# Kernel optimization log

Hardware: AMD Instinct MI355X
Metric: run time of the kernel (lower is better)

Reference implementation:

```python
import jax, jax.numpy as jnp
import numpy as np

B, N, IN_C = 8, 2048, 256
HEADS, OUT_C = 4, 128
E = 65536
BN_EPS = 1e-5


def setup_inputs() -> dict:
    key = jax.random.key(0)
    k1, k2, k3, k4 = jax.random.split(key, 4)
    x = jax.random.normal(k1, (B, N, IN_C), dtype=jnp.float32)
    edge_index = jax.random.randint(k2, (2, E), 0, N, dtype=jnp.int64)
    # Linear W: in_channels -> heads*out_channels, no bias (stored as [in, out])
    W = jax.random.normal(k3, (IN_C, HEADS * OUT_C), dtype=jnp.float32) / np.sqrt(IN_C)
    # att Linear: 2*out_channels -> 1, no bias (stored as a vector)
    a = jax.random.normal(k4, (2 * OUT_C,), dtype=jnp.float32) / np.sqrt(2 * OUT_C)
    bn_gamma = jnp.ones((OUT_C,), dtype=jnp.float32)
    bn_beta = jnp.zeros((OUT_C,), dtype=jnp.float32)
    return {"x": x, "edge_index": edge_index, "W": W, "a": a,
            "bn_gamma": bn_gamma, "bn_beta": bn_beta}


def reference(x, edge_index, W, a, bn_gamma, bn_beta):
    Bsz, Nn, _ = x.shape
    src, dst = edge_index[0], edge_index[1]
    h = (x @ W).reshape(Bsz, Nn, HEADS, OUT_C)  # [B,N,H,C]
    # att([h_src, h_dst]) == h_src @ a[:C] + h_dst @ a[C:] ; precompute per node
    s_src = jnp.einsum("bnhc,c->bnh", h, a[:OUT_C])  # [B,N,H]
    s_dst = jnp.einsum("bnhc,c->bnh", h, a[OUT_C:])
    e = s_src[:, src] + s_dst[:, dst]                 # [B,E,H]
    e = jax.nn.leaky_relu(e, negative_slope=0.2)
    e_avg = e.mean(axis=-1)                           # [B,E]
    # dense N x N attention: rows = dst, cols = src, -inf elsewhere
    attn = jnp.full((Bsz, Nn, Nn), -jnp.inf, dtype=x.dtype)
    attn = attn.at[:, dst, src].set(e_avg)
    attn = jax.nn.softmax(attn, axis=-1)
    attn = jnp.nan_to_num(attn, nan=0.0)              # rows with no edges -> 0
    # dropout is identity in eval mode
    h_flat = h.reshape(Bsz, Nn, HEADS * OUT_C)
    h_out = attn @ h_flat                             # [B,N,H*C]
    h_out = h_out.reshape(Bsz, Nn, HEADS, OUT_C).mean(axis=2)  # [B,N,C]
    # BatchNorm1d over channel dim (batch stats, biased var, affine params)
    mean = h_out.mean(axis=(0, 1))
    var = h_out.var(axis=(0, 1))
    h_out = (h_out - mean) / jnp.sqrt(var + BN_EPS) * bn_gamma + bn_beta
    return jax.nn.elu(h_out)
```

## Files before the change

### kernel.cpp

```cpp
#include <hip/hip_runtime.h>
#include <hip/hip_bf16.h>
#include <math.h>

#define BB 8
#define NN 2048
#define INC 256
#define CC 128
#define NE 65536
#define CAP 128
#define MROWS (BB*NN)
#define BN_EPS 1e-5f
#define NT 9
#define NKC 8
#define NFRAG (NT*NKC*64)

typedef unsigned int uint32;
typedef unsigned long long u64;
typedef __attribute__((ext_vector_type(8))) short short8;
typedef __attribute__((ext_vector_type(4))) float f32x4;

__device__ inline ushort f2bf(float f) {
  __hip_bfloat16 b = __float2bfloat16(f);
  return reinterpret_cast<ushort&>(b);
}
__device__ inline float bf2f(ushort h) {
  return __uint_as_float(((uint32)h) << 16);
}

__device__ inline void load_edge(const void* ei, int is64, int e, int& s, int& d) {
  if (is64) {
    const long long* p = (const long long*)ei;
    s = (int)p[e]; d = (int)p[NE + e];
  } else {
    const int* p = (const int*)ei;
    s = p[e]; d = p[NE + e];
  }
}

__global__ __launch_bounds__(256) void k_prep(const float* __restrict__ W,
                                              const float* __restrict__ a,
                                              const int* __restrict__ ei32,
                                              uint4* __restrict__ pack,
                                              int* __restrict__ flag,
                                              int* __restrict__ row_cnt) {
  __shared__ float Wl[8][520];
  __shared__ float Wms[8][132];
  __shared__ float Was[8][8];
  __shared__ float av[256];
  int m = blockIdx.x, tid = threadIdx.x;
  if (m < 8) row_cnt[m * 256 + tid] = 0;
  if (m == 0 && tid == 0) {
    int nz = 0;
    for (int t = 1; t < 128; t += 2) nz |= (ei32[t] != 0);
    *flag = nz ? 0 : 1;
  }
  av[tid] = a[tid];
  const float4* Wg = (const float4*)(W + (size_t)m * 8 * 512);
  #pragma unroll
  for (int i = 0; i < 4; ++i) {
    int idx = tid + i * 256;
    int r = idx >> 7, c4 = idx & 127;
    *(float4*)&Wl[r][c4 * 4] = Wg[idx];
  }
  __syncthreads();
  {
    int c = tid & 127, half = tid >> 7;
    #pragma unroll
    for (int ii = 0; ii < 4; ++ii) {
      int r = half * 4 + ii;
      Wms[r][c] = 0.25f * (Wl[r][c] + Wl[r][128 + c] + Wl[r][256 + c] + Wl[r][384 + c]);
    }
  }
  {
    int i8 = tid >> 5, c2 = tid & 31;
    float p[8];
    #pragma unroll
    for (int j = 0; j < 8; ++j) p[j] = 0.0f;
    #pragma unroll
    for (int t4 = 0; t4 < 4; ++t4) {
      int cc = c2 + t4 * 32;
      float asrc = av[cc], adst = av[128 + cc];
      #pragma unroll
      for (int h = 0; h < 4; ++h) {
        float w = Wl[i8][h * 128 + cc];
        p[h] += w * asrc;
        p[4 + h] += w * adst;
      }
    }
    #pragma unroll
    for (int off = 16; off > 0; off >>= 1)
      #pragma unroll
      for (int j = 0; j < 8; ++j) p[j] += __shfl_xor(p[j], off, 64);
    if (c2 < 8) Was[i8][c2] = p[c2];
  }
  __syncthreads();
  if (tid < 144) {
    int t = tid >> 4, l16 = tid & 15;
    int cch = t * 16 + l16;
    int kc = m >> 2, g = m & 3;
    uint32 h[8];
    #pragma unroll
    for (int j = 0; j < 8; ++j) {
      float v = 0.0f;
      if (cch < CC) v = Wms[j][cch];
      else if (cch < CC + 8) v = Was[j][cch - CC];
      h[j] = (uint32)f2bf(v);
    }
    uint4 u;
    u.x = h[0] | (h[1] << 16);
    u.y = h[2] | (h[3] << 16);
    u.z = h[4] | (h[5] << 16);
    u.w = h[6] | (h[7] << 16);
    pack[(t * NKC + kc) * 64 + g * 16 + l16] = u;
  }
}

__global__ __launch_bounds__(512) void k_gemm(const float* __restrict__ x,
                                              const uint4* __restrict__ pack,
                                              const void* __restrict__ ei,
                                              const int* __restrict__ flag,
                                              ushort* __restrict__ hm,
                                              float* __restrict__ s,
                                              int* __restrict__ row_cnt,
                                              int* __restrict__ row_src) {
  __shared__ uint4 lp[NFRAG];
  int tid = threadIdx.x;
  if (tid < 256) {
    int e = blockIdx.x * 256 + tid;
    int is64 = *flag;
    int src, dst;
    load_edge(ei, is64, e, src, dst);
    int pos = atomicAdd(&row_cnt[dst], 1);
    if (pos < CAP) row_src[dst * CAP + pos] = src;
  }
  #pragma unroll
  for (int i = 0; i < 9; ++i) lp[i * 512 + tid] = pack[i * 512 + tid];

  int lane = tid & 63, wv = tid >> 6;
  int rt = wv & 3, th = wv >> 2;
  int g = lane >> 4;
  int xrow = blockIdx.x * 64 + rt * 16 + (lane & 15);
  const float* xr = x + (size_t)xrow * INC;

  short8 xf[8];
  #pragma unroll
  for (int kc = 0; kc < 8; ++kc) {
    f32x4 xa = *(const f32x4*)(xr + kc * 32 + g * 8);
    f32x4 xb = *(const f32x4*)(xr + kc * 32 + g * 8 + 4);
    short8 t;
    t[0] = (short)f2bf(xa[0]); t[1] = (short)f2bf(xa[1]);
    t[2] = (short)f2bf(xa[2]); t[3] = (short)f2bf(xa[3]);
    t[4] = (short)f2bf(xb[0]); t[5] = (short)f2bf(xb[1]);
    t[6] = (short)f2bf(xb[2]); t[7] = (short)f2bf(xb[3]);
    xf[kc] = t;
  }
  __syncthreads();

  f32x4 acc[4];
  f32x4 accE = (f32x4)(0.0f);
  #pragma unroll
  for (int i = 0; i < 4; ++i) acc[i] = (f32x4)(0.0f);

  const short8* fr = (const short8*)lp;
  int tb = th * 4;
  #pragma unroll
  for (int kc = 0; kc < NKC; ++kc) {
    #pragma unroll
    for (int i = 0; i < 4; ++i) {
      short8 af = fr[((tb + i) * NKC + kc) * 64 + lane];
      acc[i] = __builtin_amdgcn_mfma_f32_16x16x32_bf16(af, xf[kc], acc[i], 0, 0, 0);
    }
    short8 ae = fr[(8 * NKC + kc) * 64 + lane];
    accE = __builtin_amdgcn_mfma_f32_16x16x32_bf16(ae, xf[kc], accE, 0, 0, 0);
  }

  ushort* hrow = hm + (size_t)xrow * CC;
  #pragma unroll
  for (int i = 0; i < 4; ++i) {
    int t = tb + i;
    uint32 p0 = (uint32)f2bf(acc[i][0]) | ((uint32)f2bf(acc[i][1]) << 16);
    uint32 p1 = (uint32)f2bf(acc[i][2]) | ((uint32)f2bf(acc[i][3]) << 16);
    *(uint2*)(hrow + t * 16 + g * 4) = make_uint2(p0, p1);
  }
  if (th == 1 && g < 2) {
    int b = xrow >> 11, n = xrow & (NN - 1);
    *(f32x4*)(s + ((size_t)n * BB + b) * 8 + g * 4) = accE;
  }
}

__global__ __launch_bounds__(256) void k_agg(const int* __restrict__ row_cnt,
                                             const int* __restrict__ row_src,
                                             const float* __restrict__ s,
                                             const uint32* __restrict__ hm32,
                                             uint32* __restrict__ hout,
                                             f32x4* __restrict__ part) {
  __shared__ int rsrc[CAP], csrc[CAP];
  __shared__ float swgt[8][CAP];
  __shared__ float emat[8][CAP];
  __shared__ float sdl[8][4];
  __shared__ f32x4 red[256];
  __shared__ uint32 bmask[64];
  __shared__ int wcnt[2];
  int d = blockIdx.x, tid = threadIdx.x;
  int lane = tid & 63, wv = tid >> 6;
  int k0 = row_cnt[d]; if (k0 > CAP) k0 = CAP;

  if (tid < 64) bmask[tid] = 0u;
  if (tid < 32) {
    int b = tid >> 2, h = tid & 3;
    sdl[b][h] = s[((size_t)d * BB + b) * 8 + 4 + h];
  }
  if (tid < k0) rsrc[tid] = row_src[d * CAP + tid];
  __syncthreads();
  int keep = 0;
  if (tid < k0) {
    int sv = rsrc[tid];
    uint32 bit = 1u << (sv & 31);
    uint32 old = atomicOr(&bmask[sv >> 5], bit);
    keep = ((old & bit) == 0) ? 1 : 0;
  }
  u64 mask = __ballot(keep);
  int pos = __popcll(mask & ((1ull << lane) - 1ull));
  if (lane == 0 && wv < 2) wcnt[wv] = (int)__popcll(mask);
  __syncthreads();
  int base = (wv == 1) ? wcnt[0] : 0;
  if (keep) csrc[base + pos] = rsrc[tid];
  __syncthreads();
  int kd = wcnt[0] + wcnt[1];
  if (tid < kd) {
    int sv = csrc[tid], r = 0;
    for (int q = 0; q < kd; ++q) r += (csrc[q] < sv) ? 1 : 0;
    rsrc[r] = sv;
  }
  __syncthreads();

  {
    int jj = tid >> 3, bb = tid & 7;
    for (int j0 = 0; j0 < kd; j0 += 32) {
      int j = j0 + jj;
      if (j < kd) {
        int r = rsrc[j];
        f32x4 ss = *(const f32x4*)(s + ((size_t)r * BB + bb) * 8);
        float sum = 0.0f;
        #pragma unroll
        for (int h = 0; h < 4; ++h) {
          float v = ss[h] + sdl[bb][h];
          sum += (v > 0.0f) ? v : 0.2f * v;
        }
        emat[bb][j] = 0.25f * sum;
      }
    }
  }
  __syncthreads();

  int b0 = wv, b1 = wv + 4;
  float v00 = (lane < kd)      ? emat[b0][lane]      : -INFINITY;
  float v01 = (lane + 64 < kd) ? emat[b0][lane + 64] : -INFINITY;
  float v10 = (lane < kd)      ? emat[b1][lane]      : -INFINITY;
  float v11 = (lane + 64 < kd) ? emat[b1][lane + 64] : -INFINITY;
  float m0 = fmaxf(v00, v01), m1 = fmaxf(v10, v11);
  #pragma unroll
  for (int off = 32; off > 0; off >>= 1) {
    m0 = fmaxf(m0, __shfl_xor(m0, off, 64));
    m1 = fmaxf(m1, __shfl_xor(m1, off, 64));
  }
  float e00 = (lane < kd)      ? expf(v00 - m0) : 0.0f;
  float e01 = (lane + 64 < kd) ? expf(v01 - m0) : 0.0f;
  float e10 = (lane < kd)      ? expf(v10 - m1) : 0.0f;
  float e11 = (lane + 64 < kd) ? expf(v11 - m1) : 0.0f;
  float sum0 = e00 + e01, sum1 = e10 + e11;
  #pragma unroll
  for (int off = 32; off > 0; off >>= 1) {
    sum0 += __shfl_xor(sum0, off, 64);
    sum1 += __shfl_xor(sum1, off, 64);
  }
  float inv0 = (kd > 0) ? 1.0f / sum0 : 0.0f;
  float inv1 = (kd > 0) ? 1.0f / sum1 : 0.0f;
  swgt[b0][lane]      = e00 * inv0;
  swgt[b0][lane + 64] = e01 * inv0;
  swgt[b1][lane]      = e10 * inv1;
  swgt[b1][lane + 64] = e11 * inv1;

  float a0 = 0.0f, a1 = 0.0f, a2 = 0.0f, a3 = 0.0f;
  const uint32* hb0 = hm32 + (size_t)b0 * NN * (CC / 2);
  const uint32* hb1 = hm32 + (size_t)b1 * NN * (CC / 2);
  #pragma unroll 4
  for (int j = 0; j < kd; ++j) {
    int r = rsrc[j];
    float w0 = swgt[b0][j], w1 = swgt[b1][j];
    uint32 u0 = hb0[(size_t)r * (CC / 2) + lane];
    uint32 u1 = hb1[(size_t)r * (CC / 2) + lane];
    a0 += w0 * bf2f((ushort)(u0 & 0xffffu));
    a1 += w0 * bf2f((ushort)(u0 >> 16));
    a2 += w1 * bf2f((ushort)(u1 & 0xffffu));
    a3 += w1 * bf2f((ushort)(u1 >> 16));
  }
  hout[((size_t)b0 * NN + d) * (CC / 2) + lane] =
      (uint32)f2bf(a0) | ((uint32)f2bf(a1) << 16);
  hout[((size_t)b1 * NN + d) * (CC / 2) + lane] =
      (uint32)f2bf(a2) | ((uint32)f2bf(a3) << 16);

  f32x4 r4;
  r4[0] = a0 + a2; r4[1] = a0 * a0 + a2 * a2;
  r4[2] = a1 + a3; r4[3] = a1 * a1 + a3 * a3;
  red[tid] = r4;
  __syncthreads();
  if (wv == 0) {
    f32x4 t = red[lane] + red[lane + 64] + red[lane + 128] + red[lane + 192];
    part[(size_t)d * 64 + lane] = t;
  }
}

__global__ __launch_bounds__(256) void k_bnred(const f32x4* __restrict__ part,
                                               const float* __restrict__ gamma,
                                               const float* __restrict__ beta,
                                               float* __restrict__ bntab) {
  __shared__ f32x4 red[256];
  int c = blockIdx.x, t = threadIdx.x;
  f32x4 acc = (f32x4)(0.0f);
  #pragma unroll
  for (int i = 0; i < 8; ++i)
    acc += part[(size_t)(t + 256 * i) * 64 + c];
  red[t] = acc;
  __syncthreads();
  for (int off = 128; off > 0; off >>= 1) {
    if (t < off) red[t] += red[t + off];
    __syncthreads();
  }
  if (t == 0) {
    f32x4 v = red[0];
    #pragma unroll
    for (int i = 0; i < 2; ++i) {
      int ch = 2 * c + i;
      float mean = v[2 * i] / (float)MROWS;
      float var  = v[2 * i + 1] / (float)MROWS - mean * mean;
      if (var < 0.0f) var = 0.0f;
      float scale = gamma[ch] / sqrtf(var + BN_EPS);
      bntab[ch] = scale;
      bntab[CC + ch] = beta[ch] - mean * scale;
    }
  }
}

__global__ __launch_bounds__(256) void k_elu(const uint32* __restrict__ hout,
                                             const float* __restrict__ bntab,
                                             float* __restrict__ out) {
  __shared__ float bsc[CC], bsh[CC];
  int tid = threadIdx.x;
  if (tid < CC) {
    bsc[tid] = bntab[tid];
    bsh[tid] = bntab[CC + tid];
  }
  __syncthreads();
  int pbase = blockIdx.x * 1024 + tid;
  #pragma unroll
  for (int i = 0; i < 4; ++i) {
    int p = pbase + i * 256;
    int cp = p & 63;
    uint32 u = hout[p];
    float y0 = bf2f((ushort)(u & 0xffffu)) * bsc[2 * cp]     + bsh[2 * cp];
    float y1 = bf2f((ushort)(u >> 16))     * bsc[2 * cp + 1] + bsh[2 * cp + 1];
    float2 o;
    o.x = (y0 > 0.0f) ? y0 : expm1f(y0);
    o.y = (y1 > 0.0f) ? y1 : expm1f(y1);
    *(float2*)(out + 2 * (size_t)p) = o;
  }
}

extern "C" void kernel_launch(void* const* d_in, const int* in_sizes, int n_in,
                              void* d_out, int out_size, void* d_ws, size_t ws_size,
                              hipStream_t stream) {
  const float* x     = (const float*)d_in[0];
  const void*  ei    = d_in[1];
  const float* W     = (const float*)d_in[2];
  const float* a     = (const float*)d_in[3];
  const float* gamma = (const float*)d_in[4];
  const float* beta  = (const float*)d_in[5];
  float* out = (float*)d_out;

  char* p = (char*)d_ws;
  ushort* hm   = (ushort*)p; p += (size_t)MROWS * CC * 2;
  uint32* hout = (uint32*)p; p += (size_t)MROWS * CC * 2;
  f32x4* part = (f32x4*)p; p += (size_t)NN * 64 * 16;
  float* s    = (float*)p; p += (size_t)MROWS * 8 * 4;
  uint4* pack = (uint4*)p; p += (size_t)NFRAG * 16;
  float* bntab = (float*)p; p += 4096;
  int* flag   = (int*)p;   p += 256;
  int* row_cnt  = (int*)p; p += NN * 4;
  int* row_src  = (int*)p; p += (size_t)NN * CAP * 4;

  k_prep<<<32, 256, 0, stream>>>(W, a, (const int*)ei, pack, flag, row_cnt);
  k_gemm<<<MROWS / 64, 512, 0, stream>>>(x, pack, ei, flag, hm, s, row_cnt, row_src);
  k_agg<<<NN, 256, 0, stream>>>(row_cnt, row_src, s, (const uint32*)hm, hout, part);
  k_bnred<<<64, 256, 0, stream>>>(part, gamma, beta, bntab);
  k_elu<<<(MROWS * CC / 2) / 1024, 256, 0, stream>>>(hout, bntab, out);
}
```

Baseline: 53.94 us.

## Rework prep to one block per W row and widen aggregation gathers to uint2

The prep kernel now launches one 128-thread block per input row of W (256 blocks instead of 32). Each block computes the head-mean and attention projections for its row and writes individual bf16 halves into the packed fragment buffer. The aggregation kernel now maps each half-wave to one batch and gathers 4 bf16 channels per lane with uint2 loads instead of 2 per lane across two batches. The BN partial-sum reduction is reorganised to match the new mapping. This aims to widen memory accesses in the gather loop and spread prep across more CUs, at the cost of scattered 2-byte stores in prep and different reduction indexing.

Result: no change. 53.43 us, median of 2 (-0.9%).

```diff
diff --git a/kernel.cpp b/kernel.cpp
--- a/kernel.cpp
+++ b/kernel.cpp
@@ -37,81 +37,48 @@
   }
 }
 
-__global__ __launch_bounds__(256) void k_prep(const float* __restrict__ W,
+__global__ __launch_bounds__(128) void k_prep(const float* __restrict__ W,
                                               const float* __restrict__ a,
                                               const int* __restrict__ ei32,
                                               uint4* __restrict__ pack,
                                               int* __restrict__ flag,
                                               int* __restrict__ row_cnt) {
-  __shared__ float Wl[8][520];
-  __shared__ float Wms[8][132];
-  __shared__ float Was[8][8];
-  __shared__ float av[256];
-  int m = blockIdx.x, tid = threadIdx.x;
-  if (m < 8) row_cnt[m * 256 + tid] = 0;
-  if (m == 0 && tid == 0) {
+  __shared__ float Wms[128];
+  __shared__ float Was[8];
+  __shared__ float red2[2][8];
+  int i = blockIdx.x, tid = threadIdx.x;
+  if (tid < 8) row_cnt[i * 8 + tid] = 0;
+  if (i == 0 && tid == 0) {
     int nz = 0;
     for (int t = 1; t < 128; t += 2) nz |= (ei32[t] != 0);
     *flag = nz ? 0 : 1;
   }
-  av[tid] = a[tid];
-  const float4* Wg = (const float4*)(W + (size_t)m * 8 * 512);
-  #pragma unroll
-  for (int i = 0; i < 4; ++i) {
-    int idx = tid + i * 256;
-    int r = idx >> 7, c4 = idx & 127;
-    *(float4*)&Wl[r][c4 * 4] = Wg[idx];
-  }
-  __syncthreads();
-  {
-    int c = tid & 127, half = tid >> 7;
-    #pragma unroll
-    for (int ii = 0; ii < 4; ++ii) {
-      int r = half * 4 + ii;
-      Wms[r][c] = 0.25f * (Wl[r][c] + Wl[r][128 + c] + Wl[r][256 + c] + Wl[r][384 + c]);
-    }
-  }
-  {
-    int i8 = tid >> 5, c2 = tid & 31;
-    float p[8];
-    #pragma unroll
-    for (int j = 0; j < 8; ++j) p[j] = 0.0f;
-    #pragma unroll
-    for (int t4 = 0; t4 < 4; ++t4) {
-      int cc = c2 + t4 * 32;
-      float asrc = av[cc], adst = av[128 + cc];
-      #pragma unroll
-      for (int h = 0; h < 4; ++h) {
-        float w = Wl[i8][h * 128 + cc];
-        p[h] += w * asrc;
-        p[4 + h] += w * adst;
-      }
-    }
-    #pragma unroll
-    for (int off = 16; off > 0; off >>= 1)
-      #pragma unroll
-      for (int j = 0; j < 8; ++j) p[j] += __shfl_xor(p[j], off, 64);
-    if (c2 < 8) Was[i8][c2] = p[c2];
-  }
-  __syncthreads();
-  if (tid < 144) {
-    int t = tid >> 4, l16 = tid & 15;
+  const float* Wr = W + (size_t)i * 512;
+  float w0 = Wr[tid], w1 = Wr[128 + tid], w2 = Wr[256 + tid], w3 = Wr[384 + tid];
+  Wms[tid] = 0.25f * (w0 + w1 + w2 + w3);
+  float asrc = a[tid], adst = a[128 + tid];
+  float p[8] = {w0 * asrc, w1 * asrc, w2 * asrc, w3 * asrc,
+                w0 * adst, w1 * adst, w2 * adst, w3 * adst};
+  #pragma unroll
+  for (int off = 32; off > 0; off >>= 1)
+    #pragma unroll
+    for (int j = 0; j < 8; ++j) p[j] += __shfl_xor(p[j], off, 64);
+  int wv = tid >> 6, lane = tid & 63;
+  if (lane == 0) {
+    #pragma unroll
+    for (int j = 0; j < 8; ++j) red2[wv][j] = p[j];
+  }
+  __syncthreads();
+  if (tid < 8) Was[tid] = red2[0][tid] + red2[1][tid];
+  __syncthreads();
+  int kc = i >> 5, gq = (i >> 3) & 3, jj = i & 7;
+  ushort* pu = (ushort*)pack;
+  for (int w = tid; w < 144; w += 128) {
+    int t = w >> 4, l16 = w & 15;
     int cch = t * 16 + l16;
-    int kc = m >> 2, g = m & 3;
-    uint32 h[8];
-    #pragma unroll
-    for (int j = 0; j < 8; ++j) {
-      float v = 0.0f;
-      if (cch < CC) v = Wms[j][cch];
-      else if (cch < CC + 8) v = Was[j][cch - CC];
-      h[j] = (uint32)f2bf(v);
-    }
-    uint4 u;
-    u.x = h[0] | (h[1] << 16);
-    u.y = h[2] | (h[3] << 16);
-    u.z = h[4] | (h[5] << 16);
-    u.w = h[6] | (h[7] << 16);
-    pack[(t * NKC + kc) * 64 + g * 16 + l16] = u;
+    float v = (cch < CC) ? Wms[cch] : ((cch < CC + 8) ? Was[cch - CC] : 0.0f);
+    int frag = (t * NKC + kc) * 64 + gq * 16 + l16;
+    pu[(size_t)frag * 8 + jj] = f2bf(v);
   }
 }
 
@@ -191,14 +158,15 @@
 __global__ __launch_bounds__(256) void k_agg(const int* __restrict__ row_cnt,
                                              const int* __restrict__ row_src,
                                              const float* __restrict__ s,
-                                             const uint32* __restrict__ hm32,
-                                             uint32* __restrict__ hout,
+                                             const uint2* __restrict__ hm2,
+                                             uint2* __restrict__ hout2,
                                              f32x4* __restrict__ part) {
   __shared__ int rsrc[CAP], csrc[CAP];
   __shared__ float swgt[8][CAP];
   __shared__ float emat[8][CAP];
   __shared__ float sdl[8][4];
-  __shared__ f32x4 red[256];
+  __shared__ f32x4 redS[256];
+  __shared__ f32x4 redQ[256];
   __shared__ uint32 bmask[64];
   __shared__ int wcnt[2];
   int d = blockIdx.x, tid = threadIdx.x;
@@ -281,33 +249,43 @@
   swgt[b1][lane]      = e10 * inv1;
   swgt[b1][lane + 64] = e11 * inv1;
 
-  float a0 = 0.0f, a1 = 0.0f, a2 = 0.0f, a3 = 0.0f;
-  const uint32* hb0 = hm32 + (size_t)b0 * NN * (CC / 2);
-  const uint32* hb1 = hm32 + (size_t)b1 * NN * (CC / 2);
+  int half = lane >> 5;
+  int bsel = wv + half * 4;
+  int cq = lane & 31;
+  const uint2* hb = hm2 + (size_t)bsel * NN * 32;
+  f32x4 a4 = (f32x4)(0.0f);
   #pragma unroll 4
   for (int j = 0; j < kd; ++j) {
     int r = rsrc[j];
-    float w0 = swgt[b0][j], w1 = swgt[b1][j];
-    uint32 u0 = hb0[(size_t)r * (CC / 2) + lane];
-    uint32 u1 = hb1[(size_t)r * (CC / 2) + lane];
-    a0 += w0 * bf2f((ushort)(u0 & 0xffffu));
-    a1 += w0 * bf2f((ushort)(u0 >> 16));
-    a2 += w1 * bf2f((ushort)(u1 & 0xffffu));
-    a3 += w1 * bf2f((ushort)(u1 >> 16));
-  }
-  hout[((size_t)b0 * NN + d) * (CC / 2) + lane] =
-      (uint32)f2bf(a0) | ((uint32)f2bf(a1) << 16);
-  hout[((size_t)b1 * NN + d) * (CC / 2) + lane] =
-      (uint32)f2bf(a2) | ((uint32)f2bf(a3) << 16);
-
-  f32x4 r4;
-  r4[0] = a0 + a2; r4[1] = a0 * a0 + a2 * a2;
-  r4[2] = a1 + a3; r4[3] = a1 * a1 + a3 * a3;
-  red[tid] = r4;
-  __syncthreads();
-  if (wv == 0) {
-    f32x4 t = red[lane] + red[lane + 64] + red[lane + 128] + red[lane + 192];
-    part[(size_t)d * 64 + lane] = t;
+    float w = swgt[bsel][j];
+    uint2 u = hb[(size_t)r * 32 + cq];
+    a4[0] += w * bf2f((ushort)(u.x & 0xffffu));
+    a4[1] += w * bf2f((ushort)(u.x >> 16));
+    a4[2] += w * bf2f((ushort)(u.y & 0xffffu));
+    a4[3] += w * bf2f((ushort)(u.y >> 16));
+  }
+  uint2 o;
+  o.x = (uint32)f2bf(a4[0]) | ((uint32)f2bf(a4[1]) << 16);
+  o.y = (uint32)f2bf(a4[2]) | ((uint32)f2bf(a4[3]) << 16);
+  hout2[((size_t)bsel * NN + d) * 32 + cq] = o;
+
+  f32x4 rq;
+  rq[0] = a4[0] * a4[0]; rq[1] = a4[1] * a4[1];
+  rq[2] = a4[2] * a4[2]; rq[3] = a4[3] * a4[3];
+  redS[tid] = a4; redQ[tid] = rq;
+  __syncthreads();
+  if (tid < 32) {
+    f32x4 ts = (f32x4)(0.0f), tq = (f32x4)(0.0f);
+    #pragma unroll
+    for (int k = 0; k < 8; ++k) {
+      int src = (k >> 1) * 64 + (k & 1) * 32 + tid;
+      ts += redS[src]; tq += redQ[src];
+    }
+    f32x4 pa, pb;
+    pa[0] = ts[0]; pa[1] = tq[0]; pa[2] = ts[1]; pa[3] = tq[1];
+    pb[0] = ts[2]; pb[1] = tq[2]; pb[2] = ts[3]; pb[3] = tq[3];
+    part[(size_t)d * 64 + 2 * tid]     = pa;
+    part[(size_t)d * 64 + 2 * tid + 1] = pb;
   }
 }
 
@@ -389,9 +367,10 @@
   int* row_cnt  = (int*)p; p += NN * 4;
   int* row_src  = (int*)p; p += (size_t)NN * CAP * 4;
 
-  k_prep<<<32, 256, 0, stream>>>(W, a, (const int*)ei, pack, flag, row_cnt);
+  k_prep<<<INC, 128, 0, stream>>>(W, a, (const int*)ei, pack, flag, row_cnt);
   k_gemm<<<MROWS / 64, 512, 0, stream>>>(x, pack, ei, flag, hm, s, row_cnt, row_src);
-  k_agg<<<NN, 256, 0, stream>>>(row_cnt, row_src, s, (const uint32*)hm, hout, part);
+  k_agg<<<NN, 256, 0, stream>>>(row_cnt, row_src, s, (const uint2*)hm,
+                                (uint2*)hout, part);
   k_bnred<<<64, 256, 0, stream>>>(part, gamma, beta, bntab);
   k_elu<<<(MROWS * CC / 2) / 1024, 256, 0, stream>>>(hout, bntab, out);
 }
```
